# Optimization experiments

Measured on AMD Instinct MI355X. Metric: run time of the kernel, lower is better.

The kernel has to match this reference:

```python
import jax, jax.numpy as jnp
from jax import lax
import numpy as np

K = 2000      # self.k: entries kept per sample
T_SC = 3      # number of IHT iterations
DN = ('NCHW', 'OIHW', 'NCHW')


def keep_k_largest(X, k):
    # Per-sample hard threshold: keep the k largest-magnitude entries of the
    # flattened [C,H,W] activations, zero the rest (exactly k kept, as in argsort).
    B = X.shape[0]
    flat = X.reshape(B, -1)                                # [B, N]
    _, idx = lax.top_k(jnp.abs(flat), k)                   # [B, k]
    vals = jnp.take_along_axis(flat, idx, axis=1)          # [B, k]
    out = jnp.zeros_like(flat).at[jnp.arange(B)[:, None], idx].set(vals)
    return out.reshape(X.shape)


def _D_apply(X, W_D):
    # ConvTranspose2d(numb_atom -> dp_channels), stride 1, no padding:
    # full correlation with the spatially flipped, io-swapped kernel.
    kh, kw = W_D.shape[2], W_D.shape[3]
    Wt = jnp.flip(jnp.transpose(W_D, (1, 0, 2, 3)), (2, 3))  # [dp, atoms, kh, kw]
    return lax.conv_general_dilated(X, Wt, (1, 1),
                                    [(kh - 1, kh - 1), (kw - 1, kw - 1)],
                                    dimension_numbers=DN)


def _Dt_apply(Z, W_D):
    # Conv2d(dp_channels -> numb_atom) VALID; D_trans.weight = D.weight.permute(0,1,3,2)
    Wt = jnp.transpose(W_D, (0, 1, 3, 2))                  # [atoms, dp, kh, kw]
    return lax.conv_general_dilated(Z, Wt, (1, 1), 'VALID', dimension_numbers=DN)


def setup_inputs() -> dict:
    key = jax.random.key(0)
    k1, k2, k3 = jax.random.split(key, 3)
    Y = jax.random.normal(k1, (32, 3, 64, 64), jnp.float32)
    X0 = jax.random.normal(k2, (32, 128, 57, 57), jnp.float32)   # random init X in forward
    W_D = jax.random.normal(k3, (128, 3, 8, 8), jnp.float32) * 0.05
    return {"Y": Y, "X0": X0, "W_D": W_D}


def reference(Y, X0, W_D):
    # HT_arg = X - D_trans(D(X) - Y); then T_SC hard-threshold iterations.
    HT_arg = X0 - _Dt_apply(_D_apply(X0, W_D) - Y, W_D)
    X = HT_arg
    for i in range(T_SC):
        X = keep_k_largest(HT_arg, K)
        if i < T_SC - 1:  # final HT_arg update in the original is unused
            HT_arg = X - _Dt_apply(_D_apply(X, W_D) - Y, W_D)
    return X
```

## Files before the change

### kernel.cpp

```cpp
#include <hip/hip_runtime.h>

#define BATCH 32
#define ATOMS 128
#define CCH 3
#define XH 57
#define XW 57
#define OHH 64
#define OWW 64
#define KSEL 2000
#define PIX (XH*XW)
#define NPS (ATOMS*PIX)
#define NTOT (BATCH*NPS)
#define RPS (CCH*OHH*OWW)
#define RTOT (BATCH*RPS)
#define CANDCAP 32768
#define NW 24576
#define WSEG 102

__global__ __launch_bounds__(256) void prep_k(const float* __restrict__ Wg,
    double* __restrict__ WDd, double* __restrict__ Wt2d,
    const float* __restrict__ Y, double* __restrict__ Rd) {
  int e = blockIdx.x * 256 + threadIdx.x;
  if (e < NW) {
    {
      int kw = e & 7; int t = e >> 3; int c = t % 3; t /= 3; int kh = t & 7; int a = t >> 3;
      WDd[e] = (double)Wg[(a*3 + c)*64 + kh*8 + kw];
    }
    {
      int a = e & 127; int t = e >> 7; int j = t & 7; int i = (t >> 3) & 7; int c = t >> 6;
      Wt2d[e] = (double)Wg[(a*3 + c)*64 + j*8 + i];
    }
  }
  if (e < RTOT) Rd[e] = -(double)Y[e];
}

__global__ __launch_bounds__(256) void convD_k(const float* __restrict__ X,
    const double* __restrict__ WDd, double* __restrict__ Rd) {
  __shared__ float Xs[8][11][72];
  int p = blockIdx.x;
  int lg = (p & 7) * 256 + (p >> 3);
  int b = lg >> 6; int rem = lg & 63;
  int band = rem >> 2, quarter = rem & 3;
  int row0 = band * 4;
  int a_base = quarter * 32;
  int tid = threadIdx.x;
  int ox = tid & 63;
  int wv = __builtin_amdgcn_readfirstlane(tid >> 6);
  const float* Xb = X + (size_t)b * NPS;

  double acc[4][3];
#pragma unroll
  for (int ty = 0; ty < 4; ++ty)
#pragma unroll
    for (int c = 0; c < 3; ++c) acc[ty][c] = 0.0;

  for (int ch = 0; ch < 4; ++ch) {
    __syncthreads();
    for (int e = tid; e < 8 * 11 * 72; e += 256) {
      int ai = e / 792; int rem2 = e - ai * 792;
      int r = rem2 / 72; int ss = rem2 - r * 72;
      int gy = row0 - 7 + r;
      int xcol = ss - 7;
      int a = a_base + ch * 8 + ai;
      float v = 0.0f;
      if ((unsigned)xcol < (unsigned)XW && (unsigned)gy < (unsigned)XH)
        v = Xb[a * PIX + gy * XW + xcol];
      Xs[ai][r][ss] = v;
    }
    __syncthreads();
#pragma unroll
    for (int jj = 0; jj < 2; ++jj) {
      int ai = (wv << 1) + jj;
      int a  = a_base + ch * 8 + ai;
      const double* Wa = WDd + a * 192;
#pragma unroll
      for (int r = 0; r < 11; ++r) {
        int gy = row0 - 7 + r;
        if ((unsigned)gy >= (unsigned)XH) continue;
        double xd[8];
#pragma unroll
        for (int t = 0; t < 8; ++t) xd[t] = (double)Xs[ai][r][ox + t];
#pragma unroll
        for (int ty = 0; ty < 4; ++ty) {
          int kh = ty + 7 - r;
          if ((unsigned)kh < 8u) {
            const double* Wk = Wa + kh * 24;
#pragma unroll
            for (int kw = 0; kw < 8; ++kw) {
              acc[ty][0] = fma(xd[7 - kw], Wk[kw],      acc[ty][0]);
              acc[ty][1] = fma(xd[7 - kw], Wk[8 + kw],  acc[ty][1]);
              acc[ty][2] = fma(xd[7 - kw], Wk[16 + kw], acc[ty][2]);
            }
          }
        }
      }
    }
  }
#pragma unroll
  for (int ty = 0; ty < 4; ++ty) {
    int oy = row0 + ty;
#pragma unroll
    for (int c = 0; c < 3; ++c)
      atomicAdd(&Rd[((size_t)(b * CCH + c) << 12) + (oy << 6) + ox], acc[ty][c]);
  }
}

__global__ __launch_bounds__(256) void convD_sparse_k(const float* __restrict__ Wg,
    const int* __restrict__ nzidx, const float* __restrict__ nzval,
    const float* __restrict__ Y, float* __restrict__ R) {
  __shared__ double accd[512];
  __shared__ float Wf[8192];
  __shared__ int   li[KSEL];
  __shared__ float lv[KSEL];
  int p = blockIdx.x;
  int lg = (p & 7) * 96 + (p >> 3);
  int s = lg / 24; int r = lg % 24; int c = r >> 3; int band = r & 7;
  int row0 = band * 8;
  int tid = threadIdx.x;
  for (int e = tid; e < 512; e += 256) accd[e] = 0.0;
  for (int e = tid; e < 8192; e += 256) {
    int a = e >> 6, k2 = e & 63;
    Wf[e] = Wg[(a * 3 + c) * 64 + k2];
  }
  for (int e = tid; e < KSEL; e += 256) {
    li[e] = nzidx[s * KSEL + e];
    lv[e] = nzval[s * KSEL + e];
  }
  __syncthreads();
  int slot = tid >> 3, kw = tid & 7;
  for (int e = slot; e < KSEL; e += 32) {
    int idx = li[e];
    int a = (int)((unsigned)idx / 3249u);
    int pp = idx - a * 3249;
    int y = (int)((unsigned)pp / 57u);
    int x = pp - y * 57;
    int dy = y - row0;
    if (dy < -7 || dy > 7) continue;
    double val = (double)lv[e];
    const float* wp = Wf + (a << 6) + kw;
#pragma unroll
    for (int kh = 0; kh < 8; ++kh) {
      int rr = dy + kh;
      if ((unsigned)rr < 8u)
        __hip_atomic_fetch_add(&accd[(rr << 6) + x + kw],
                               val * (double)wp[kh << 3],
                               __ATOMIC_RELAXED, __HIP_MEMORY_SCOPE_WORKGROUP);
    }
  }
  __syncthreads();
  const float* Yb = Y + (((size_t)(s * CCH + c)) << 12) + (row0 << 6);
  float* Rb = R + (((size_t)(s * CCH + c)) << 12) + (row0 << 6);
  for (int e = tid; e < 512; e += 256)
    Rb[e] = (float)(accd[e] - (double)Yb[e]);
}

template <typename TR, bool SPX>
__global__ __launch_bounds__(256) void convDt_k(const TR* __restrict__ R,
    const double* __restrict__ Wt2d, const float* __restrict__ Xprev,
    const int* __restrict__ nzidx, const float* __restrict__ nzval,
    float* __restrict__ HT, unsigned* __restrict__ g1) {
  __shared__ float Rl[3][15][72];
  __shared__ unsigned hh[1024];
  __shared__ float Xp[8][8][XW];
  int p = blockIdx.x;
  int lg = (p & 7) * 512 + (p >> 3);
  int b = lg >> 7; int rem = lg & 127; int ag = rem >> 3; int by = rem & 7;
  int row0 = by * 8;
  int a0 = ag * 8;
  int tid = threadIdx.x;
  for (int e = tid; e < 1024; e += 256) hh[e] = 0;
  for (int e = tid; e < 3 * 15 * 72; e += 256) {
    int c = e / (15 * 72); int r2 = e - c * (15 * 72);
    int rr = r2 / 72; int cc = r2 - rr * 72;
    int gr = row0 + rr;
    float v = 0.0f;
    if (cc < OWW && gr < OHH)
      v = (float)R[((size_t)(b * CCH + c) << 12) + (gr << 6) + cc];
    Rl[c][rr][cc] = v;
  }
  if constexpr (SPX) {
    for (int e = tid; e < 8 * 8 * XW; e += 256) (&Xp[0][0][0])[e] = 0.0f;
    __syncthreads();
    for (int e = tid; e < KSEL; e += 256) {
      int idx = nzidx[b * KSEL + e];
      int a = (int)((unsigned)idx / 3249u);
      int pp2 = idx - a * 3249;
      int yy = (int)((unsigned)pp2 / 57u);
      int xx = pp2 - yy * 57;
      if ((unsigned)(a - a0) < 8u && (unsigned)(yy - row0) < 8u)
        Xp[a - a0][yy - row0][xx] = nzval[b * KSEL + e];
    }
  }
  __syncthreads();
  int x = tid & 63, yg = tid >> 6;
  int yb = yg * 2;
  double acc[8][2];
#pragma unroll
  for (int aa = 0; aa < 8; ++aa) { acc[aa][0] = 0.0; acc[aa][1] = 0.0; }

#pragma unroll 1
  for (int c = 0; c < 3; ++c) {
#pragma unroll 1
    for (int j = 0; j < 8; ++j) {
      double rw[9];
#pragma unroll
      for (int r = 0; r < 9; ++r) rw[r] = (double)Rl[c][yb + r][x + j];
#pragma unroll
      for (int i = 0; i < 8; ++i) {
        const double* wp = Wt2d + ((c * 8 + i) * 8 + j) * 128 + a0;
#pragma unroll
        for (int aa = 0; aa < 8; ++aa) {
          double w = wp[aa];
          acc[aa][0] = fma(rw[i + 0], w, acc[aa][0]);
          acc[aa][1] = fma(rw[i + 1], w, acc[aa][1]);
        }
      }
    }
  }
  if (x < XW) {
#pragma unroll
    for (int ty = 0; ty < 2; ++ty) {
      int yy = row0 + yb + ty;
      if (yy < XH) {
#pragma unroll
        for (int aa = 0; aa < 8; ++aa) {
          size_t xo = (size_t)(b * ATOMS + a0 + aa) * PIX + yy * XW + x;
          double xprev;
          if constexpr (SPX) xprev = (double)Xp[aa][yb + ty][x];
          else               xprev = (double)Xprev[xo];
          float fv = (float)(xprev - acc[aa][ty]);
          HT[xo] = fv;
          unsigned u = __float_as_uint(fv) & 0x7fffffffu;
          unsigned bin = u >> 20;
          atomicAdd(&hh[bin >> 1], 1u << ((bin & 1) << 4));
        }
      }
    }
  }
  __syncthreads();
  unsigned* gp = g1 + (size_t)b * 2048;
  for (int e = tid; e < 1024; e += 256) {
    unsigned v = hh[e];
    unsigned lo = v & 0xffffu, hi = v >> 16;
    if (lo) atomicAdd(&gp[2 * e], lo);
    if (hi) atomicAdd(&gp[2 * e + 1], hi);
  }
}

__global__ __launch_bounds__(256) void hist2_k(const float* __restrict__ HT,
    const unsigned* __restrict__ g1, unsigned* __restrict__ g2,
    int* __restrict__ cand, int* __restrict__ candcnt) {
  __shared__ unsigned h[1024];
  __shared__ unsigned part[256];
  __shared__ int lidx[4096];
  __shared__ int lcnt, lbase, b1_sh;
  int tid = threadIdx.x;
  int s = blockIdx.x >> 5;
  int chunk = blockIdx.x & 31;
  const unsigned* hg1 = g1 + (size_t)s * 2048;
  unsigned psum = 0;
#pragma unroll
  for (int e = 0; e < 8; ++e) psum += hg1[tid * 8 + e];
  part[tid] = psum;
  for (int e = tid; e < 1024; e += 256) h[e] = 0;
  if (tid == 0) lcnt = 0;
  __syncthreads();
  if (tid == 0) {
    int Kv = KSEL;
    unsigned cumBefore = 0;
    int bsel = 0;
    for (int q = 255; q >= 0; --q) {
      unsigned ps = part[q];
      if ((int)(cumBefore + ps) >= Kv) {
        for (int e = q * 8 + 7;; --e) {
          unsigned c2 = cumBefore + hg1[e];
          if ((int)c2 >= Kv) { bsel = e; break; }
          cumBefore = c2;
        }
        break;
      }
      cumBefore += ps;
    }
    b1_sh = bsel;
  }
  __syncthreads();
  unsigned pre = (unsigned)b1_sh;
  const uint4* U4 = (const uint4*)(HT + (size_t)s * NPS);
  for (int i4 = chunk * 256 + tid; i4 < NPS / 4; i4 += 32 * 256) {
    uint4 v = U4[i4];
    unsigned uu[4] = {v.x, v.y, v.z, v.w};
#pragma unroll
    for (int t = 0; t < 4; ++t) {
      unsigned u = uu[t] & 0x7fffffffu;
      if ((u >> 20) == pre) {
        atomicAdd(&h[(u >> 10) & 1023], 1u);
        int pos = atomicAdd(&lcnt, 1);
        if (pos < 4096) lidx[pos] = i4 * 4 + t;
      }
    }
  }
  __syncthreads();
  if (tid == 0) {
    int n = lcnt < 4096 ? lcnt : 4096;
    lbase = atomicAdd(&candcnt[s], n);
  }
  __syncthreads();
  int n = lcnt < 4096 ? lcnt : 4096;
  int base = lbase;
  for (int e = tid; e < n; e += 256) {
    int g = base + e;
    if (g < CANDCAP) cand[s * CANDCAP + g] = lidx[e];
  }
  for (int e = tid; e < 1024; e += 256)
    if (h[e]) atomicAdd(&g2[s * 1024 + e], h[e]);
}

__global__ __launch_bounds__(256) void pass3_k(const float* __restrict__ HT,
    const int* __restrict__ cand, const int* __restrict__ candcnt,
    const unsigned* __restrict__ g1, const unsigned* __restrict__ g2,
    unsigned* __restrict__ tau_out, int* __restrict__ cutoff_out) {
  int s = blockIdx.x;
  __shared__ unsigned h[1024];
  __shared__ unsigned part[256];
  __shared__ int eqidx[1024];
  __shared__ int eqn;
  __shared__ unsigned tau_sh;
  __shared__ int k3_sh;
  __shared__ int b1_sh, k1_sh, b2_sh, k2_sh;
  int t = threadIdx.x;
  const unsigned* hg1 = g1 + (size_t)s * 2048;
  unsigned s1 = 0;
#pragma unroll
  for (int e = 0; e < 8; ++e) s1 += hg1[t * 8 + e];
  part[t] = s1;
  for (int e = t; e < 1024; e += 256) h[e] = 0;
  if (t == 0) eqn = 0;
  __syncthreads();
  if (t == 0) {
    int Kv = KSEL;
    unsigned cumBefore = 0;
    int bsel = 0;
    for (int q = 255; q >= 0; --q) {
      unsigned ps = part[q];
      if ((int)(cumBefore + ps) >= Kv) {
        for (int e = q * 8 + 7;; --e) {
          unsigned c2 = cumBefore + hg1[e];
          if ((int)c2 >= Kv) { bsel = e; break; }
          cumBefore = c2;
        }
        break;
      }
      cumBefore += ps;
    }
    b1_sh = bsel;
    k1_sh = Kv - (int)cumBefore;
  }
  __syncthreads();
  const unsigned* hg = g2 + s * 1024;
  unsigned s2 = 0;
#pragma unroll
  for (int e = 0; e < 4; ++e) s2 += hg[t * 4 + e];
  part[t] = s2;
  __syncthreads();
  if (t == 0) {
    int Kv = k1_sh;
    unsigned cumBefore = 0;
    int bsel = 0;
    for (int q = 255; q >= 0; --q) {
      unsigned ps = part[q];
      if ((int)(cumBefore + ps) >= Kv) {
        for (int e = q * 4 + 3;; --e) {
          unsigned c2 = cumBefore + hg[e];
          if ((int)c2 >= Kv) { bsel = e; break; }
          cumBefore = c2;
        }
        break;
      }
      cumBefore += ps;
    }
    b2_sh = bsel;
    k2_sh = Kv - (int)cumBefore;
  }
  __syncthreads();
  int n = candcnt[s];
  if (n > CANDCAP) n = CANDCAP;
  unsigned pre21 = (((unsigned)b1_sh) << 10) | (unsigned)b2_sh;
  const unsigned* U = (const unsigned*)(HT + (size_t)s * NPS);
  for (int e = t; e < n; e += 256) {
    int i = cand[s * CANDCAP + e];
    unsigned u = U[i] & 0x7fffffffu;
    if ((u >> 10) == pre21) atomicAdd(&h[u & 1023], 1u);
  }
  __syncthreads();
  if (t == 0) {
    int Kv = k2_sh;
    unsigned cumBefore = 0;
    int b3 = 0;
    for (int e = 1023; e >= 0; --e) {
      unsigned c2 = cumBefore + h[e];
      if ((int)c2 >= Kv) { b3 = e; break; }
      cumBefore = c2;
    }
    tau_sh = (pre21 << 10) | (unsigned)b3;
    k3_sh = Kv - (int)cumBefore;
  }
  __syncthreads();
  unsigned tau = tau_sh;
  for (int e = t; e < n; e += 256) {
    int i = cand[s * CANDCAP + e];
    unsigned u = U[i] & 0x7fffffffu;
    if (u == tau) {
      int pos = atomicAdd(&eqn, 1);
      if (pos < 1024) eqidx[pos] = i;
    }
  }
  __syncthreads();
  if (t == 0) {
    int m = eqn < 1024 ? eqn : 1024;
    int k3 = k3_sh;
    int cutoff;
    if (k3 >= m) {
      cutoff = 0x7fffffff;
    } else {
      int last = -1;
      for (int r = 0; r < k3; ++r) {
        int mn = 0x7fffffff;
        for (int q = 0; q < m; ++q) {
          int v = eqidx[q];
          if (v > last && v < mn) mn = v;
        }
        last = mn;
      }
      cutoff = last;
    }
    tau_out[s] = tau;
    cutoff_out[s] = cutoff;
  }
}

__global__ __launch_bounds__(256) void write_k(const float* __restrict__ HT,
    const unsigned* __restrict__ tau, const int* __restrict__ cutoff,
    float* __restrict__ Xo, int* __restrict__ nzidx, float* __restrict__ nzval,
    int* __restrict__ nzcnt, int store_x) {
  __shared__ int lidx[2048];
  __shared__ float lval[2048];
  __shared__ int lcnt, lbase;
  int s = blockIdx.x / WSEG;
  int seg = blockIdx.x % WSEG;
  int tid = threadIdx.x;
  bool emit = (nzidx != nullptr);
  if (tid == 0) lcnt = 0;
  __syncthreads();
  unsigned tt = tau[s];
  int co = cutoff[s];
  size_t sbase = (size_t)s * NPS;
  const float4* H4 = (const float4*)(HT + sbase);
  float4* X4 = (float4*)(Xo + sbase);
  int f0 = seg * 1024;
#pragma unroll
  for (int rr = 0; rr < 4; ++rr) {
    int i4 = f0 + rr * 256 + tid;
    if (i4 < NPS / 4) {
      float4 v = H4[i4];
      float vv[4] = {v.x, v.y, v.z, v.w};
      float oo[4];
#pragma unroll
      for (int t = 0; t < 4; ++t) {
        int il = i4 * 4 + t;
        unsigned u = __float_as_uint(vv[t]) & 0x7fffffffu;
        bool keep = (u > tt) || (u == tt && il <= co);
        oo[t] = keep ? vv[t] : 0.0f;
        if (keep && emit) {
          int pos = atomicAdd(&lcnt, 1);
          if (pos < 2048) { lidx[pos] = il; lval[pos] = vv[t]; }
        }
      }
      if (store_x) X4[i4] = make_float4(oo[0], oo[1], oo[2], oo[3]);
    }
  }
  if (!emit) return;
  __syncthreads();
  if (tid == 0) lbase = atomicAdd(&nzcnt[s], lcnt);
  __syncthreads();
  int n = lcnt < 2048 ? lcnt : 2048;
  int base = lbase;
  for (int e = tid; e < n; e += 256) {
    int g = base + e;
    if (g < KSEL) { nzidx[s * KSEL + g] = lidx[e]; nzval[s * KSEL + g] = lval[e]; }
  }
}

extern "C" void kernel_launch(void* const* d_in, const int* in_sizes, int n_in,
                              void* d_out, int out_size, void* d_ws, size_t ws_size,
                              hipStream_t stream) {
  const float* Y  = (const float*)d_in[0];
  const float* X0 = (const float*)d_in[1];
  const float* Wg = (const float*)d_in[2];
  float* Xout = (float*)d_out;

  double* WDd  = (double*)d_ws;
  double* Wt2d = WDd + NW;
  float* HT   = (float*)(Wt2d + NW);
  float* Rbuf = HT + NTOT;
  double* Rd  = (double*)(Rbuf + RTOT);
  unsigned* g1 = (unsigned*)(Rd + RTOT);
  unsigned* g2 = g1 + 32 * 2048;
  int* candcnt = (int*)(g2 + 32 * 1024);
  int* nzcnt = candcnt + 32;
  unsigned* tau = (unsigned*)(nzcnt + 32);
  int* cutoff = (int*)(tau + 32);
  int* cand = cutoff + 32;
  int* nzidx = cand + 32 * CANDCAP;
  float* nzval = (float*)(nzidx + 32 * KSEL);
  size_t zero_bytes = (size_t)(32 * 2048 + 32 * 1024 + 32 + 32) * 4;

  prep_k<<<dim3((RTOT + 255) / 256), dim3(256), 0, stream>>>(Wg, WDd, Wt2d, Y, Rd);

  for (int it = 0; it < 3; ++it) {
    hipMemsetAsync(g1, 0, zero_bytes, stream);
    if (it == 0) {
      convD_k<<<dim3(2048), dim3(256), 0, stream>>>(X0, WDd, Rd);
      convDt_k<double, false><<<dim3(4096), dim3(256), 0, stream>>>(
          Rd, Wt2d, X0, nullptr, nullptr, HT, g1);
    } else {
      convD_sparse_k<<<dim3(BATCH * CCH * 8), dim3(256), 0, stream>>>(
          Wg, nzidx, nzval, Y, Rbuf);
      convDt_k<float, true><<<dim3(4096), dim3(256), 0, stream>>>(
          Rbuf, Wt2d, nullptr, nzidx, nzval, HT, g1);
    }
    hist2_k<<<dim3(BATCH * 32), dim3(256), 0, stream>>>(HT, g1, g2, cand, candcnt);
    pass3_k<<<dim3(BATCH), dim3(256), 0, stream>>>(HT, cand, candcnt, g1, g2, tau, cutoff);
    bool last = (it == 2);
    write_k<<<dim3(BATCH * WSEG), dim3(256), 0, stream>>>(HT, tau, cutoff, Xout,
        last ? nullptr : nzidx, last ? nullptr : nzval, nzcnt, last ? 1 : 0);
  }
}
```

Baseline: 1.031 ms.

## Replace memsets with in-kernel zeroing, read dense X in convDt, double LDS in convD

The per-iteration hipMemsetAsync is removed. The histogram and counter buffers are now zeroed inside prep_k, write_k and pass3_k, which saves launch and memset overhead. convDt no longer scatters the sparse nonzero list into shared memory; instead write_k always stores the dense thresholded X and convDt reads it as Xprev. This trades the in-block scatter for extra global writes and reads of the full activation tensor. convD also stages its input tile as double in shared memory, with 4 atoms per chunk instead of 8, to avoid repeated float-to-double conversions at the cost of more chunks and barriers.

```diff
diff --git a/kernel.cpp b/kernel.cpp
--- a/kernel.cpp
+++ b/kernel.cpp
@@ -16,10 +16,12 @@
 #define CANDCAP 32768
 #define NW 24576
 #define WSEG 102
+#define ZWORDS (32*2048 + 32*1024)
 
 __global__ __launch_bounds__(256) void prep_k(const float* __restrict__ Wg,
     double* __restrict__ WDd, double* __restrict__ Wt2d,
-    const float* __restrict__ Y, double* __restrict__ Rd) {
+    const float* __restrict__ Y, double* __restrict__ Rd,
+    unsigned* __restrict__ zbuf) {
   int e = blockIdx.x * 256 + threadIdx.x;
   if (e < NW) {
     {
@@ -32,11 +34,12 @@
     }
   }
   if (e < RTOT) Rd[e] = -(double)Y[e];
+  if (e < ZWORDS + 64) zbuf[e] = 0;
 }
 
 __global__ __launch_bounds__(256) void convD_k(const float* __restrict__ X,
     const double* __restrict__ WDd, double* __restrict__ Rd) {
-  __shared__ float Xs[8][11][72];
+  __shared__ double Xs[4][11][72];
   int p = blockIdx.x;
   int lg = (p & 7) * 256 + (p >> 3);
   int b = lg >> 6; int rem = lg & 63;
@@ -54,24 +57,22 @@
 #pragma unroll
     for (int c = 0; c < 3; ++c) acc[ty][c] = 0.0;
 
-  for (int ch = 0; ch < 4; ++ch) {
+  for (int ch = 0; ch < 8; ++ch) {
     __syncthreads();
-    for (int e = tid; e < 8 * 11 * 72; e += 256) {
+    for (int e = tid; e < 4 * 11 * 72; e += 256) {
       int ai = e / 792; int rem2 = e - ai * 792;
       int r = rem2 / 72; int ss = rem2 - r * 72;
       int gy = row0 - 7 + r;
       int xcol = ss - 7;
-      int a = a_base + ch * 8 + ai;
+      int a = a_base + ch * 4 + ai;
       float v = 0.0f;
       if ((unsigned)xcol < (unsigned)XW && (unsigned)gy < (unsigned)XH)
         v = Xb[a * PIX + gy * XW + xcol];
-      Xs[ai][r][ss] = v;
+      Xs[ai][r][ss] = (double)v;
     }
     __syncthreads();
-#pragma unroll
-    for (int jj = 0; jj < 2; ++jj) {
-      int ai = (wv << 1) + jj;
-      int a  = a_base + ch * 8 + ai;
+    {
+      int a = a_base + ch * 4 + wv;
       const double* Wa = WDd + a * 192;
 #pragma unroll
       for (int r = 0; r < 11; ++r) {
@@ -79,7 +80,7 @@
         if ((unsigned)gy >= (unsigned)XH) continue;
         double xd[8];
 #pragma unroll
-        for (int t = 0; t < 8; ++t) xd[t] = (double)Xs[ai][r][ox + t];
+        for (int t = 0; t < 8; ++t) xd[t] = Xs[wv][r][ox + t];
 #pragma unroll
         for (int ty = 0; ty < 4; ++ty) {
           int kh = ty + 7 - r;
@@ -154,14 +155,12 @@
     Rb[e] = (float)(accd[e] - (double)Yb[e]);
 }
 
-template <typename TR, bool SPX>
+template <typename TR>
 __global__ __launch_bounds__(256) void convDt_k(const TR* __restrict__ R,
     const double* __restrict__ Wt2d, const float* __restrict__ Xprev,
-    const int* __restrict__ nzidx, const float* __restrict__ nzval,
     float* __restrict__ HT, unsigned* __restrict__ g1) {
   __shared__ float Rl[3][15][72];
   __shared__ unsigned hh[1024];
-  __shared__ float Xp[8][8][XW];
   int p = blockIdx.x;
   int lg = (p & 7) * 512 + (p >> 3);
   int b = lg >> 7; int rem = lg & 127; int ag = rem >> 3; int by = rem & 7;
@@ -178,19 +177,6 @@
       v = (float)R[((size_t)(b * CCH + c) << 12) + (gr << 6) + cc];
     Rl[c][rr][cc] = v;
   }
-  if constexpr (SPX) {
-    for (int e = tid; e < 8 * 8 * XW; e += 256) (&Xp[0][0][0])[e] = 0.0f;
-    __syncthreads();
-    for (int e = tid; e < KSEL; e += 256) {
-      int idx = nzidx[b * KSEL + e];
-      int a = (int)((unsigned)idx / 3249u);
-      int pp2 = idx - a * 3249;
-      int yy = (int)((unsigned)pp2 / 57u);
-      int xx = pp2 - yy * 57;
-      if ((unsigned)(a - a0) < 8u && (unsigned)(yy - row0) < 8u)
-        Xp[a - a0][yy - row0][xx] = nzval[b * KSEL + e];
-    }
-  }
   __syncthreads();
   int x = tid & 63, yg = tid >> 6;
   int yb = yg * 2;
@@ -225,10 +211,7 @@
 #pragma unroll
         for (int aa = 0; aa < 8; ++aa) {
           size_t xo = (size_t)(b * ATOMS + a0 + aa) * PIX + yy * XW + x;
-          double xprev;
-          if constexpr (SPX) xprev = (double)Xp[aa][yb + ty][x];
-          else               xprev = (double)Xprev[xo];
-          float fv = (float)(xprev - acc[aa][ty]);
+          float fv = (float)((double)Xprev[xo] - acc[aa][ty]);
           HT[xo] = fv;
           unsigned u = __float_as_uint(fv) & 0x7fffffffu;
           unsigned bin = u >> 20;
@@ -316,9 +299,10 @@
 }
 
 __global__ __launch_bounds__(256) void pass3_k(const float* __restrict__ HT,
-    const int* __restrict__ cand, const int* __restrict__ candcnt,
+    const int* __restrict__ cand, int* __restrict__ candcnt,
     const unsigned* __restrict__ g1, const unsigned* __restrict__ g2,
-    unsigned* __restrict__ tau_out, int* __restrict__ cutoff_out) {
+    int* __restrict__ nzcnt, unsigned* __restrict__ tau_out,
+    int* __restrict__ cutoff_out) {
   int s = blockIdx.x;
   __shared__ unsigned h[1024];
   __shared__ unsigned part[256];
@@ -435,13 +419,15 @@
     }
     tau_out[s] = tau;
     cutoff_out[s] = cutoff;
+    candcnt[s] = 0;
+    nzcnt[s] = 0;
   }
 }
 
 __global__ __launch_bounds__(256) void write_k(const float* __restrict__ HT,
     const unsigned* __restrict__ tau, const int* __restrict__ cutoff,
     float* __restrict__ Xo, int* __restrict__ nzidx, float* __restrict__ nzval,
-    int* __restrict__ nzcnt, int store_x) {
+    int* __restrict__ nzcnt, unsigned* __restrict__ zbuf) {
   __shared__ int lidx[2048];
   __shared__ float lval[2048];
   __shared__ int lcnt, lbase;
@@ -449,6 +435,10 @@
   int seg = blockIdx.x % WSEG;
   int tid = threadIdx.x;
   bool emit = (nzidx != nullptr);
+  if (zbuf) {
+    int e = blockIdx.x * 256 + tid;
+    if (e < ZWORDS) zbuf[e] = 0;
+  }
   if (tid == 0) lcnt = 0;
   __syncthreads();
   unsigned tt = tau[s];
@@ -475,7 +465,7 @@
           if (pos < 2048) { lidx[pos] = il; lval[pos] = vv[t]; }
         }
       }
-      if (store_x) X4[i4] = make_float4(oo[0], oo[1], oo[2], oo[3]);
+      X4[i4] = make_float4(oo[0], oo[1], oo[2], oo[3]);
     }
   }
   if (!emit) return;
@@ -512,26 +502,25 @@
   int* cand = cutoff + 32;
   int* nzidx = cand + 32 * CANDCAP;
   float* nzval = (float*)(nzidx + 32 * KSEL);
-  size_t zero_bytes = (size_t)(32 * 2048 + 32 * 1024 + 32 + 32) * 4;
-
-  prep_k<<<dim3((RTOT + 255) / 256), dim3(256), 0, stream>>>(Wg, WDd, Wt2d, Y, Rd);
+
+  prep_k<<<dim3((RTOT + 255) / 256), dim3(256), 0, stream>>>(Wg, WDd, Wt2d, Y, Rd, g1);
 
   for (int it = 0; it < 3; ++it) {
-    hipMemsetAsync(g1, 0, zero_bytes, stream);
+    const float* Xsrc = (it == 0) ? X0 : (const float*)Xout;
     if (it == 0) {
-      convD_k<<<dim3(2048), dim3(256), 0, stream>>>(X0, WDd, Rd);
-      convDt_k<double, false><<<dim3(4096), dim3(256), 0, stream>>>(
-          Rd, Wt2d, X0, nullptr, nullptr, HT, g1);
+      convD_k<<<dim3(2048), dim3(256), 0, stream>>>(Xsrc, WDd, Rd);
+      convDt_k<double><<<dim3(4096), dim3(256), 0, stream>>>(Rd, Wt2d, Xsrc, HT, g1);
     } else {
       convD_sparse_k<<<dim3(BATCH * CCH * 8), dim3(256), 0, stream>>>(
           Wg, nzidx, nzval, Y, Rbuf);
-      convDt_k<float, true><<<dim3(4096), dim3(256), 0, stream>>>(
-          Rbuf, Wt2d, nullptr, nzidx, nzval, HT, g1);
+      convDt_k<float><<<dim3(4096), dim3(256), 0, stream>>>(Rbuf, Wt2d, Xsrc, HT, g1);
     }
     hist2_k<<<dim3(BATCH * 32), dim3(256), 0, stream>>>(HT, g1, g2, cand, candcnt);
-    pass3_k<<<dim3(BATCH), dim3(256), 0, stream>>>(HT, cand, candcnt, g1, g2, tau, cutoff);
+    pass3_k<<<dim3(BATCH), dim3(256), 0, stream>>>(HT, cand, candcnt, g1, g2,
+                                                   nzcnt, tau, cutoff);
     bool last = (it == 2);
     write_k<<<dim3(BATCH * WSEG), dim3(256), 0, stream>>>(HT, tau, cutoff, Xout,
-        last ? nullptr : nzidx, last ? nullptr : nzval, nzcnt, last ? 1 : 0);
-  }
-}
+        last ? nullptr : nzidx, last ? nullptr : nzval, nzcnt,
+        last ? nullptr : g1);
+  }
+}
```

After: 1.020 ms. Within noise of the previous version (-1.1%).
